# Performance work log

Measured on AMD Instinct MI355X. Metric: run time of the kernel, lower is better.

## Reference

```python
import jax, jax.numpy as jnp
import numpy as np

N_NODES = 100000
N_EDGES = 1600000
IN_DIM = 256
HID = 128
OUT_DIM = 2
N_LAYERS = 4
BN_EPS = 1e-5


def setup_inputs() -> dict:
    key = jax.random.key(0)
    ks = jax.random.split(key, 10)
    s_in = 1.0 / np.sqrt(IN_DIM)
    s_h = 1.0 / np.sqrt(HID)
    return {
        "x": jax.random.normal(ks[0], (N_NODES, IN_DIM), dtype=jnp.float32),
        "edge_index": jax.random.randint(ks[1], (2, N_EDGES), 0, N_NODES, dtype=jnp.int32),
        "W_in": jax.random.normal(ks[2], (IN_DIM, HID), dtype=jnp.float32) * s_in,
        "b_in": jnp.zeros((HID,), dtype=jnp.float32),
        # SAGEConv per-layer weights: lin_l (aggregated neighbors), lin_r (self/root)
        "W_l": jax.random.normal(ks[3], (N_LAYERS, HID, HID), dtype=jnp.float32) * s_h,
        "b_l": jnp.zeros((N_LAYERS, HID), dtype=jnp.float32),
        "W_r": jax.random.normal(ks[4], (N_LAYERS, HID, HID), dtype=jnp.float32) * s_h,
        "b_r": jnp.zeros((N_LAYERS, HID), dtype=jnp.float32),
        # BatchNorm (eval mode) params/buffers
        "bn_gamma": jnp.ones((N_LAYERS, HID), dtype=jnp.float32),
        "bn_beta": jnp.zeros((N_LAYERS, HID), dtype=jnp.float32),
        "bn_mean": jax.random.normal(ks[5], (N_LAYERS, HID), dtype=jnp.float32) * 0.01,
        "bn_var": jnp.ones((N_LAYERS, HID), dtype=jnp.float32),
        "W_cls": jax.random.normal(ks[6], (HID, OUT_DIM), dtype=jnp.float32) * s_h,
        "b_cls": jnp.zeros((OUT_DIM,), dtype=jnp.float32),
    }


def _sage_mean(h, src, dst, n):
    # gather source-node features along edges, scatter-mean at targets
    msg = h[src]  # [E, HID] -- the large irregular gather
    agg = jax.ops.segment_sum(msg, dst, num_segments=n)  # [N, HID]
    cnt = jax.ops.segment_sum(jnp.ones((src.shape[0],), h.dtype), dst, num_segments=n)
    return agg / jnp.maximum(cnt, 1.0)[:, None]


def reference(x, edge_index, W_in, b_in, W_l, b_l, W_r, b_r,
              bn_gamma, bn_beta, bn_mean, bn_var, W_cls, b_cls):
    n = x.shape[0]
    src, dst = edge_index[0], edge_index[1]
    h = jax.nn.relu(x @ W_in + b_in)  # dropout is identity at eval
    for i in range(N_LAYERS):
        h_in = h
        mean = _sage_mean(h, src, dst, n)
        h = mean @ W_l[i] + b_l[i] + h @ W_r[i] + b_r[i]
        # BatchNorm1d in eval mode (running stats)
        h = bn_gamma[i] * (h - bn_mean[i]) * jax.lax.rsqrt(bn_var[i] + BN_EPS) + bn_beta[i]
        h = jax.nn.relu(h)
        h = h + h_in
    return jax.nn.log_softmax(h @ W_cls + b_cls, axis=1)
```

## Files before the change

### kernel.cpp

```cpp
#include <hip/hip_runtime.h>

typedef unsigned int uint;
typedef unsigned short ushort;
typedef __attribute__((ext_vector_type(8))) short short8v;
typedef __attribute__((ext_vector_type(4))) float f32x4;

#define IN_DIM 256
#define HID 128
#define BN_EPS 1e-5f
#define NSHARD 8

__device__ __forceinline__ float bf2f(ushort u) { return __uint_as_float(((uint)u) << 16); }
__device__ __forceinline__ ushort f2bf(float f) {
    uint u = __float_as_uint(f);
    return (ushort)((u + 0x7fffu + ((u >> 16) & 1u)) >> 16);
}
__device__ __forceinline__ uint cvt_pk_bf16(float a, float b) {
    uint r;
    asm("v_cvt_pk_bf16_f32 %0, %1, %2" : "=v"(r) : "v"(a), "v"(b));
    return r;
}
__device__ __forceinline__ void gload_lds16(const void* g, void* l) {
    __builtin_amdgcn_global_load_lds(
        (const __attribute__((address_space(1))) uint*)g,
        (__attribute__((address_space(3))) uint*)l, 16, 0, 0);
}


__global__ void count_deg_kernel(const int* __restrict__ ei, int* __restrict__ deg, int E) {
    int e = blockIdx.x * blockDim.x + threadIdx.x;
    if (e < E) atomicAdd(&deg[ei[E + e]], 1);
}

#define SCAN_THREADS 256
#define SCAN_ELEMS 1024

__global__ __launch_bounds__(SCAN_THREADS) void scan1_kernel(const int* __restrict__ deg,
                                                             int* __restrict__ outp,
                                                             int* __restrict__ bsum, int n) {
    __shared__ int sdata[SCAN_THREADS];
    int t = threadIdx.x;
    int base = blockIdx.x * SCAN_ELEMS + t * 4;
    int v0 = 0, v1 = 0, v2 = 0, v3 = 0;
    if (base + 0 < n) v0 = deg[base + 0];
    if (base + 1 < n) v1 = deg[base + 1];
    if (base + 2 < n) v2 = deg[base + 2];
    if (base + 3 < n) v3 = deg[base + 3];
    int s = v0 + v1 + v2 + v3;
    sdata[t] = s;
    __syncthreads();
    int val = s;
    for (int off = 1; off < SCAN_THREADS; off <<= 1) {
        int add = (t >= off) ? sdata[t - off] : 0;
        __syncthreads();
        val += add;
        sdata[t] = val;
        __syncthreads();
    }
    int excl = val - s;
    if (base + 0 < n) outp[base + 0] = excl;
    if (base + 1 < n) outp[base + 1] = excl + v0;
    if (base + 2 < n) outp[base + 2] = excl + v0 + v1;
    if (base + 3 < n) outp[base + 3] = excl + v0 + v1 + v2;
    if (t == SCAN_THREADS - 1) bsum[blockIdx.x] = val;
}

__global__ void scan2_kernel(int* bsum, int nb) {
    if (threadIdx.x == 0 && blockIdx.x == 0) {
        int acc = 0;
        for (int i = 0; i < nb; i++) { int v = bsum[i]; bsum[i] = acc; acc += v; }
        bsum[nb] = acc;
    }
}

__global__ void scan3_kernel(int* __restrict__ row_ptr, const int* __restrict__ bsum, int n, int nb) {
    int i = blockIdx.x * blockDim.x + threadIdx.x;
    if (i < n) row_ptr[i] += bsum[i >> 10];
    else if (i == n) row_ptr[n] = bsum[nb];
}

__global__ __launch_bounds__(256) void fill_csr_sharded(const int* __restrict__ ei,
                                                        int* __restrict__ cursor,
                                                        int* __restrict__ esrc,
                                                        int E, int shardSize) {
    int s = blockIdx.x & (NSHARD - 1);
    int rank = blockIdx.x >> 3;
    int nteam = gridDim.x >> 3;
    int lo = s * shardSize;
    int hi = lo + shardSize;
    int stride = nteam * blockDim.x;
    for (int e = rank * blockDim.x + threadIdx.x; e < E; e += stride) {
        int d = ei[E + e];
        if (d >= lo && d < hi) {
            int pos = atomicAdd(&cursor[d], 1);
            esrc[pos] = ei[e];
        }
    }
}


__global__ __launch_bounds__(256) void pack_win(const float* __restrict__ W, ushort* __restrict__ Wt) {
    int idx = blockIdx.x * 256 + threadIdx.x;
    int k = idx >> 7, c = idx & 127;
    Wt[c * IN_DIM + k] = f2bf(W[idx]);
}

__global__ __launch_bounds__(256) void pack_wcat(const float* __restrict__ Wl,
                                                 const float* __restrict__ Wr,
                                                 ushort* __restrict__ Wt) {
    int idx = blockIdx.x * 256 + threadIdx.x;
    int layer = idx >> 15;
    int rem = idx & 32767;
    int k = rem >> 7, c = rem & 127;
    float v = (k < HID) ? Wl[layer * HID * HID + k * HID + c]
                        : Wr[layer * HID * HID + (k - HID) * HID + c];
    Wt[layer * (HID * 256) + c * 256 + k] = f2bf(v);
}


__global__ __launch_bounds__(256) void sage_mean_bf16(const ushort* __restrict__ h,
                                                      const int* __restrict__ row_ptr,
                                                      const int* __restrict__ esrc,
                                                      ushort* __restrict__ meanb, int n) {
    int node = blockIdx.x * 4 + (threadIdx.x >> 6);
    if (node >= n) return;
    int lane = threadIdx.x & 63;
    int start = row_ptr[node];
    int end = row_ptr[node + 1];
    float ax = 0.f, ay = 0.f;
    int j = start;
    for (; j + 15 < end; j += 16) {
        uint v[16];
        #pragma unroll
        for (int q = 0; q < 16; q++)
            v[q] = *(const uint*)(h + (size_t)esrc[j + q] * HID + lane * 2);
        #pragma unroll
        for (int q = 0; q < 16; q++) {
            ax += bf2f((ushort)(v[q] & 0xffffu));
            ay += bf2f((ushort)(v[q] >> 16));
        }
    }
    for (; j + 7 < end; j += 8) {
        uint v[8];
        #pragma unroll
        for (int q = 0; q < 8; q++)
            v[q] = *(const uint*)(h + (size_t)esrc[j + q] * HID + lane * 2);
        #pragma unroll
        for (int q = 0; q < 8; q++) {
            ax += bf2f((ushort)(v[q] & 0xffffu));
            ay += bf2f((ushort)(v[q] >> 16));
        }
    }
    for (; j < end; ++j) {
        uint v0 = *(const uint*)(h + (size_t)esrc[j] * HID + lane * 2);
        ax += bf2f((ushort)(v0 & 0xffffu));
        ay += bf2f((ushort)(v0 >> 16));
    }
    int deg = end - start;
    float inv = 1.0f / (float)(deg > 1 ? deg : 1);
    uint o = (uint)f2bf(ax * inv) | (((uint)f2bf(ay * inv)) << 16);
    *(uint*)(meanb + (size_t)node * HID + lane * 2) = o;
}


__global__ __launch_bounds__(256) void input_gemm_mfma(const float* __restrict__ x,
                                                       const ushort* __restrict__ Wt,
                                                       const float* __restrict__ b,
                                                       ushort* __restrict__ hout, int n) {
    __shared__ float Axs[32 * IN_DIM];
    int t = threadIdx.x;
    int l = t & 63;
    int wv = t >> 6;
    int colbase = wv * 32;
    int lr = l & 15;
    int grp = l >> 4;
    int ko = grp * 8;

    short8v Bf[8][2];
    #pragma unroll
    for (int ks = 0; ks < 8; ks++) {
        #pragma unroll
        for (int nt = 0; nt < 2; nt++) {
            int c = colbase + nt * 16 + lr;
            Bf[ks][nt] = *(const short8v*)(Wt + (size_t)c * IN_DIM + ks * 32 + ko);
        }
    }
    float bias0 = b[colbase + lr];
    float bias1 = b[colbase + 16 + lr];

    int ntiles = (n + 31) >> 5;
    for (int tile = blockIdx.x; tile < ntiles; tile += gridDim.x) {
        int row0 = tile * 32;
        __syncthreads();
        {
            const char* xb = (const char*)(x + (size_t)row0 * IN_DIM);
            char* lb = (char*)Axs;
            #pragma unroll
            for (int i = 0; i < 8; i++) {
                int off = i * 4096 + t * 16;
                int src = off ^ (((off >> 10) & 7) << 4);
                gload_lds16(xb + src, lb + i * 4096 + wv * 1024);
            }
        }
        __syncthreads();
        f32x4 acc00 = {0.f,0.f,0.f,0.f}, acc01 = {0.f,0.f,0.f,0.f};
        f32x4 acc10 = {0.f,0.f,0.f,0.f}, acc11 = {0.f,0.f,0.f,0.f};
        #pragma unroll
        for (int m = 0; m < 2; m++) {
            int r = m * 16 + lr;
            int rswz = (r & 7) << 4;
            const char* rowp = (const char*)Axs + r * 1024;
            short8v Af[8];
            #pragma unroll
            for (int ks = 0; ks < 8; ks++) {
                int kb = (ko + ks * 32) * 4;
                float4 p = *(const float4*)(rowp + (kb ^ rswz));
                float4 q = *(const float4*)(rowp + ((kb + 16) ^ rswz));
                union { uint4 u; short8v s; } cv;
                cv.u.x = cvt_pk_bf16(p.x, p.y);
                cv.u.y = cvt_pk_bf16(p.z, p.w);
                cv.u.z = cvt_pk_bf16(q.x, q.y);
                cv.u.w = cvt_pk_bf16(q.z, q.w);
                Af[ks] = cv.s;
            }
            if (m == 0) {
                #pragma unroll
                for (int ks = 0; ks < 8; ks++) {
                    acc00 = __builtin_amdgcn_mfma_f32_16x16x32_bf16(Af[ks], Bf[ks][0], acc00, 0, 0, 0);
                    acc01 = __builtin_amdgcn_mfma_f32_16x16x32_bf16(Af[ks], Bf[ks][1], acc01, 0, 0, 0);
                }
            } else {
                #pragma unroll
                for (int ks = 0; ks < 8; ks++) {
                    acc10 = __builtin_amdgcn_mfma_f32_16x16x32_bf16(Af[ks], Bf[ks][0], acc10, 0, 0, 0);
                    acc11 = __builtin_amdgcn_mfma_f32_16x16x32_bf16(Af[ks], Bf[ks][1], acc11, 0, 0, 0);
                }
            }
        }
        #pragma unroll
        for (int m = 0; m < 2; m++) {
            int rbase = row0 + m * 16 + grp * 4;
            f32x4 a0 = m == 0 ? acc00 : acc10;
            f32x4 a1 = m == 0 ? acc01 : acc11;
            #pragma unroll
            for (int r = 0; r < 4; r++) {
                int rowd = rbase + r;
                if (rowd < n) {
                    float z0 = a0[r] + bias0; z0 = z0 > 0.f ? z0 : 0.f;
                    float z1 = a1[r] + bias1; z1 = z1 > 0.f ? z1 : 0.f;
                    hout[(size_t)rowd * HID + colbase + lr] = f2bf(z0);
                    hout[(size_t)rowd * HID + colbase + 16 + lr] = f2bf(z1);
                }
            }
        }
    }
}


__global__ __launch_bounds__(256) void sage_layer_mfma(const ushort* __restrict__ h,
                                                       const ushort* __restrict__ mh,
                                                       ushort* __restrict__ hout,
                                                       const ushort* __restrict__ Wt,
                                                       const float* __restrict__ bl,
                                                       const float* __restrict__ br,
                                                       const float* __restrict__ gamma,
                                                       const float* __restrict__ beta,
                                                       const float* __restrict__ bmean,
                                                       const float* __restrict__ bvar,
                                                       int n) {
    __shared__ ushort Ams[64 * HID];
    __shared__ ushort Ahs[64 * HID];
    int t = threadIdx.x;
    int l = t & 63;
    int wv = t >> 6;
    int colbase = wv * 32;
    int lr = l & 15;
    int grp = l >> 4;
    int ko = grp * 8;

    short8v Bf[8][2];
    #pragma unroll
    for (int ks = 0; ks < 8; ks++) {
        #pragma unroll
        for (int nt = 0; nt < 2; nt++) {
            int c = colbase + nt * 16 + lr;
            Bf[ks][nt] = *(const short8v*)(Wt + (size_t)c * 256 + ks * 32 + ko);
        }
    }
    int c0 = colbase + lr;
    int c1 = c0 + 16;
    float scale0 = gamma[c0] * rsqrtf(bvar[c0] + BN_EPS);
    float scale1 = gamma[c1] * rsqrtf(bvar[c1] + BN_EPS);
    float shift0 = beta[c0] + (bl[c0] + br[c0] - bmean[c0]) * scale0;
    float shift1 = beta[c1] + (bl[c1] + br[c1] - bmean[c1]) * scale1;

    int ntiles = (n + 63) >> 6;
    for (int tile = blockIdx.x; tile < ntiles; tile += gridDim.x) {
        int row0 = tile * 64;
        __syncthreads();
        {
            const char* mb = (const char*)(mh + (size_t)row0 * HID);
            const char* hb = (const char*)(h + (size_t)row0 * HID);
            char* lm = (char*)Ams;
            char* lh = (char*)Ahs;
            #pragma unroll
            for (int i = 0; i < 4; i++) {
                int off = i * 4096 + t * 16;
                int src = off ^ (((off >> 8) & 7) << 4);
                gload_lds16(mb + src, lm + i * 4096 + wv * 1024);
                gload_lds16(hb + src, lh + i * 4096 + wv * 1024);
            }
        }
        __syncthreads();
        #pragma unroll
        for (int m = 0; m < 4; m++) {
            int r = m * 16 + lr;
            int rswz = (r & 7) << 4;
            const char* mrow = (const char*)Ams + r * 256;
            const char* hrow = (const char*)Ahs + r * 256;
            short8v Af[8];
            #pragma unroll
            for (int ks = 0; ks < 4; ks++) {
                int kb = (ko + ks * 32) * 2;
                Af[ks] = *(const short8v*)(mrow + (kb ^ rswz));
            }
            #pragma unroll
            for (int ks = 4; ks < 8; ks++) {
                int kb = (ko + (ks - 4) * 32) * 2;
                Af[ks] = *(const short8v*)(hrow + (kb ^ rswz));
            }
            f32x4 acc0 = {0.f,0.f,0.f,0.f};
            f32x4 acc1 = {0.f,0.f,0.f,0.f};
            #pragma unroll
            for (int ks = 0; ks < 8; ks++) {
                acc0 = __builtin_amdgcn_mfma_f32_16x16x32_bf16(Af[ks], Bf[ks][0], acc0, 0, 0, 0);
                acc1 = __builtin_amdgcn_mfma_f32_16x16x32_bf16(Af[ks], Bf[ks][1], acc1, 0, 0, 0);
            }
            int rbase = m * 16 + grp * 4;
            #pragma unroll
            for (int r2 = 0; r2 < 4; r2++) {
                int rloc = rbase + r2;
                int rowd = row0 + rloc;
                if (rowd < n) {
                    int rs = (rloc & 7) << 4;
                    float res0 = bf2f(*(const ushort*)((const char*)Ahs + rloc * 256 + ((c0 * 2) ^ rs)));
                    float res1 = bf2f(*(const ushort*)((const char*)Ahs + rloc * 256 + ((c1 * 2) ^ rs)));
                    float z0 = acc0[r2] * scale0 + shift0; z0 = z0 > 0.f ? z0 : 0.f;
                    float z1 = acc1[r2] * scale1 + shift1; z1 = z1 > 0.f ? z1 : 0.f;
                    hout[(size_t)rowd * HID + c0] = f2bf(z0 + res0);
                    hout[(size_t)rowd * HID + c1] = f2bf(z1 + res1);
                }
            }
        }
    }
}


__global__ __launch_bounds__(256) void classifier_bf16(const ushort* __restrict__ h,
                                                       const float* __restrict__ Wc,
                                                       const float* __restrict__ bc,
                                                       float* __restrict__ outp, int n) {
    __shared__ float Wcs[HID * 2];
    int t = threadIdx.x;
    if (t < 64) *(float4*)&Wcs[t * 4] = *(const float4*)&Wc[t * 4];
    __syncthreads();
    int rowInBlk = t >> 4;
    int sub = t & 15;
    int row = blockIdx.x * 16 + rowInBlk;
    float l0 = 0.f, l1 = 0.f;
    if (row < n) {
        const ushort* hr = h + (size_t)row * HID + sub * 8;
        uint4 v = *(const uint4*)hr;
        float e0 = bf2f((ushort)(v.x & 0xffffu)), e1 = bf2f((ushort)(v.x >> 16));
        float e2 = bf2f((ushort)(v.y & 0xffffu)), e3 = bf2f((ushort)(v.y >> 16));
        float e4 = bf2f((ushort)(v.z & 0xffffu)), e5 = bf2f((ushort)(v.z >> 16));
        float e6 = bf2f((ushort)(v.w & 0xffffu)), e7 = bf2f((ushort)(v.w >> 16));
        int k0 = sub * 8;
        l0 += e0 * Wcs[(k0 + 0) * 2] + e1 * Wcs[(k0 + 1) * 2] + e2 * Wcs[(k0 + 2) * 2] + e3 * Wcs[(k0 + 3) * 2];
        l0 += e4 * Wcs[(k0 + 4) * 2] + e5 * Wcs[(k0 + 5) * 2] + e6 * Wcs[(k0 + 6) * 2] + e7 * Wcs[(k0 + 7) * 2];
        l1 += e0 * Wcs[(k0 + 0) * 2 + 1] + e1 * Wcs[(k0 + 1) * 2 + 1] + e2 * Wcs[(k0 + 2) * 2 + 1] + e3 * Wcs[(k0 + 3) * 2 + 1];
        l1 += e4 * Wcs[(k0 + 4) * 2 + 1] + e5 * Wcs[(k0 + 5) * 2 + 1] + e6 * Wcs[(k0 + 6) * 2 + 1] + e7 * Wcs[(k0 + 7) * 2 + 1];
    }
    #pragma unroll
    for (int off = 1; off < 16; off <<= 1) {
        l0 += __shfl_xor(l0, off);
        l1 += __shfl_xor(l1, off);
    }
    if (sub == 0 && row < n) {
        l0 += bc[0];
        l1 += bc[1];
        float m = fmaxf(l0, l1);
        float lse = m + logf(expf(l0 - m) + expf(l1 - m));
        outp[(size_t)row * 2 + 0] = l0 - lse;
        outp[(size_t)row * 2 + 1] = l1 - lse;
    }
}


extern "C" void kernel_launch(void* const* d_in, const int* in_sizes, int n_in,
                              void* d_out, int out_size, void* d_ws, size_t ws_size,
                              hipStream_t stream) {
    const float* x     = (const float*)d_in[0];
    const int*   ei    = (const int*)d_in[1];
    const float* W_in  = (const float*)d_in[2];
    const float* b_in  = (const float*)d_in[3];
    const float* W_l   = (const float*)d_in[4];
    const float* b_l   = (const float*)d_in[5];
    const float* W_r   = (const float*)d_in[6];
    const float* b_r   = (const float*)d_in[7];
    const float* bn_g  = (const float*)d_in[8];
    const float* bn_b  = (const float*)d_in[9];
    const float* bn_m  = (const float*)d_in[10];
    const float* bn_v  = (const float*)d_in[11];
    const float* W_cls = (const float*)d_in[12];
    const float* b_cls = (const float*)d_in[13];
    float* outp = (float*)d_out;

    const int N = in_sizes[0] / IN_DIM;
    const int E = in_sizes[1] / 2;

    char* w = (char*)d_ws;
    const size_t HB = (size_t)N * HID * sizeof(ushort);
    ushort* hA     = (ushort*)(w);
    ushort* hB     = (ushort*)(w + HB);
    ushort* meanb  = (ushort*)(w + 2 * HB);
    ushort* Wt_in  = (ushort*)(w + 3 * HB);
    ushort* WcatT  = (ushort*)(w + 3 * HB + 65536);
    char*  ints    = w + 3 * HB + 65536 + 262144;
    int*   row_ptr = (int*)(ints);
    int*   cursor  = (int*)(ints + 400128);
    int*   bsum    = (int*)(ints + 800256);
    int*   esrc    = (int*)(ints + 801280);

    const int nbScan = (N + SCAN_ELEMS - 1) / SCAN_ELEMS;
    const int shardSize = (N + NSHARD - 1) / NSHARD;

    pack_win<<<128, 256, 0, stream>>>(W_in, Wt_in);
    pack_wcat<<<512, 256, 0, stream>>>(W_l, W_r, WcatT);

    hipMemsetAsync(cursor, 0, (size_t)N * sizeof(int), stream);
    count_deg_kernel<<<(E + 255) / 256, 256, 0, stream>>>(ei, cursor, E);
    scan1_kernel<<<nbScan, SCAN_THREADS, 0, stream>>>(cursor, row_ptr, bsum, N);
    scan2_kernel<<<1, 64, 0, stream>>>(bsum, nbScan);
    scan3_kernel<<<(N + 256) / 256, 256, 0, stream>>>(row_ptr, bsum, N, nbScan);
    hipMemcpyAsync(cursor, row_ptr, (size_t)N * sizeof(int), hipMemcpyDeviceToDevice, stream);
    fill_csr_sharded<<<2048, 256, 0, stream>>>(ei, cursor, esrc, E, shardSize);

    input_gemm_mfma<<<(N + 31) / 32, 256, 0, stream>>>(x, Wt_in, b_in, hA, N);

    ushort* hcur = hA;
    ushort* hoth = hB;
    for (int i = 0; i < 4; i++) {
        sage_mean_bf16<<<(N + 3) / 4, 256, 0, stream>>>(hcur, row_ptr, esrc, meanb, N);
        sage_layer_mfma<<<(N + 63) / 64, 256, 0, stream>>>(hcur, meanb, hoth,
                                                  WcatT + (size_t)i * HID * 256,
                                                  b_l + i * HID, b_r + i * HID,
                                                  bn_g + i * HID, bn_b + i * HID,
                                                  bn_m + i * HID, bn_v + i * HID, N);
        ushort* tmp = hcur; hcur = hoth; hoth = tmp;
    }

    classifier_bf16<<<(N + 15) / 16, 256, 0, stream>>>(hcur, W_cls, b_cls, outp, N);
}
```

Measured before the change: 580.4 us.

## Replace atomic CSR build with two-level bucketed counting sort

The CSR construction no longer uses global degree atomics, a three-kernel scan, a memcpy and a sharded atomic fill. It now histograms destinations into 512-node buckets per edge chunk, scans those counts in one block, and partitions edges into buckets with LDS atomics. Each bucket then builds its own row_ptr slice and sorted source list in shared memory. The aim is fewer global atomics and launches and more local scatter, at the cost of an extra 8-byte-per-edge staging buffer, a single-block serial scan over 256 chunks, and a different within-row edge order.

```diff
diff --git a/kernel.cpp b/kernel.cpp
--- a/kernel.cpp
+++ b/kernel.cpp
@@ -8,7 +8,6 @@
 #define IN_DIM 256
 #define HID 128
 #define BN_EPS 1e-5f
-#define NSHARD 8
 
 __device__ __forceinline__ float bf2f(ushort u) { return __uint_as_float(((uint)u) << 16); }
 __device__ __forceinline__ ushort f2bf(float f) {
@@ -27,73 +26,121 @@
 }
 
 
-__global__ void count_deg_kernel(const int* __restrict__ ei, int* __restrict__ deg, int E) {
-    int e = blockIdx.x * blockDim.x + threadIdx.x;
-    if (e < E) atomicAdd(&deg[ei[E + e]], 1);
-}
-
-#define SCAN_THREADS 256
-#define SCAN_ELEMS 1024
-
-__global__ __launch_bounds__(SCAN_THREADS) void scan1_kernel(const int* __restrict__ deg,
-                                                             int* __restrict__ outp,
-                                                             int* __restrict__ bsum, int n) {
-    __shared__ int sdata[SCAN_THREADS];
-    int t = threadIdx.x;
-    int base = blockIdx.x * SCAN_ELEMS + t * 4;
-    int v0 = 0, v1 = 0, v2 = 0, v3 = 0;
-    if (base + 0 < n) v0 = deg[base + 0];
-    if (base + 1 < n) v1 = deg[base + 1];
-    if (base + 2 < n) v2 = deg[base + 2];
-    if (base + 3 < n) v3 = deg[base + 3];
-    int s = v0 + v1 + v2 + v3;
-    sdata[t] = s;
-    __syncthreads();
-    int val = s;
-    for (int off = 1; off < SCAN_THREADS; off <<= 1) {
-        int add = (t >= off) ? sdata[t - off] : 0;
-        __syncthreads();
-        val += add;
-        sdata[t] = val;
-        __syncthreads();
-    }
-    int excl = val - s;
-    if (base + 0 < n) outp[base + 0] = excl;
-    if (base + 1 < n) outp[base + 1] = excl + v0;
-    if (base + 2 < n) outp[base + 2] = excl + v0 + v1;
-    if (base + 3 < n) outp[base + 3] = excl + v0 + v1 + v2;
-    if (t == SCAN_THREADS - 1) bsum[blockIdx.x] = val;
-}
-
-__global__ void scan2_kernel(int* bsum, int nb) {
-    if (threadIdx.x == 0 && blockIdx.x == 0) {
-        int acc = 0;
-        for (int i = 0; i < nb; i++) { int v = bsum[i]; bsum[i] = acc; acc += v; }
-        bsum[nb] = acc;
-    }
-}
-
-__global__ void scan3_kernel(int* __restrict__ row_ptr, const int* __restrict__ bsum, int n, int nb) {
-    int i = blockIdx.x * blockDim.x + threadIdx.x;
-    if (i < n) row_ptr[i] += bsum[i >> 10];
-    else if (i == n) row_ptr[n] = bsum[nb];
-}
-
-__global__ __launch_bounds__(256) void fill_csr_sharded(const int* __restrict__ ei,
-                                                        int* __restrict__ cursor,
-                                                        int* __restrict__ esrc,
-                                                        int E, int shardSize) {
-    int s = blockIdx.x & (NSHARD - 1);
-    int rank = blockIdx.x >> 3;
-    int nteam = gridDim.x >> 3;
-    int lo = s * shardSize;
-    int hi = lo + shardSize;
-    int stride = nteam * blockDim.x;
-    for (int e = rank * blockDim.x + threadIdx.x; e < E; e += stride) {
-        int d = ei[E + e];
-        if (d >= lo && d < hi) {
-            int pos = atomicAdd(&cursor[d], 1);
-            esrc[pos] = ei[e];
+__global__ __launch_bounds__(256) void hist_kernel(const int* __restrict__ ei,
+                                                   int* __restrict__ histG,
+                                                   int E, int chunk) {
+    __shared__ int hcnt[256];
+    int t = threadIdx.x;
+    hcnt[t] = 0;
+    __syncthreads();
+    int e0 = blockIdx.x * chunk;
+    int e1 = min(E, e0 + chunk);
+    for (int e = e0 + t; e < e1; e += 256)
+        atomicAdd(&hcnt[__builtin_nontemporal_load(ei + E + e) >> 9], 1);
+    __syncthreads();
+    histG[blockIdx.x * 256 + t] = hcnt[t];
+}
+
+__global__ __launch_bounds__(256) void basescan_kernel(const int* __restrict__ histG,
+                                                       int* __restrict__ baseG,
+                                                       int* __restrict__ bucketStart,
+                                                       int nchunk, int nbuck, int E) {
+    __shared__ int sA[256], sB[256];
+    int t = threadIdx.x;
+    int tot = 0;
+    for (int c = 0; c < nchunk; c++) tot += histG[c * 256 + t];
+    sA[t] = tot;
+    __syncthreads();
+    int* src = sA; int* dst = sB;
+    for (int off = 1; off < 256; off <<= 1) {
+        int v = src[t];
+        if (t >= off) v += src[t - off];
+        dst[t] = v;
+        __syncthreads();
+        int* tmp = src; src = dst; dst = tmp;
+    }
+    int excl = src[t] - tot;
+    if (t < nbuck) bucketStart[t] = excl;
+    if (t == 0) bucketStart[nbuck] = E;
+    int running = excl;
+    for (int c = 0; c < nchunk; c++) {
+        baseG[c * 256 + t] = running;
+        running += histG[c * 256 + t];
+    }
+}
+
+__global__ __launch_bounds__(256) void partition_kernel(const int* __restrict__ ei,
+                                                        const int* __restrict__ baseG,
+                                                        uint2* __restrict__ ebuck,
+                                                        int E, int chunk) {
+    __shared__ int cur[256];
+    int t = threadIdx.x;
+    cur[t] = baseG[blockIdx.x * 256 + t];
+    __syncthreads();
+    int e0 = blockIdx.x * chunk;
+    int e1 = min(E, e0 + chunk);
+    for (int e = e0 + t; e < e1; e += 256) {
+        int d = __builtin_nontemporal_load(ei + E + e);
+        int s = __builtin_nontemporal_load(ei + e);
+        int pos = atomicAdd(&cur[d >> 9], 1);
+        ebuck[pos] = make_uint2((uint)s, (uint)d);
+    }
+}
+
+__global__ __launch_bounds__(256) void bucket_build(const uint2* __restrict__ ebuck,
+                                                    const int* __restrict__ bucketStart,
+                                                    int* __restrict__ row_ptr,
+                                                    int* __restrict__ esrc,
+                                                    int n, int nbuck) {
+    __shared__ int deg[512];
+    __shared__ int sA[512], sB[512];
+    __shared__ int cur[512];
+    __shared__ int img[16384];
+    int b = blockIdx.x;
+    int t = threadIdx.x;
+    int lo = b << 9;
+    int hi = min(n, lo + 512);
+    int nn = hi - lo;
+    int eStart = bucketStart[b];
+    int eEnd = bucketStart[b + 1];
+    int cnt = eEnd - eStart;
+    for (int i = t; i < 512; i += 256) deg[i] = 0;
+    __syncthreads();
+    for (int e = eStart + t; e < eEnd; e += 256) {
+        uint2 p = ebuck[e];
+        atomicAdd(&deg[(int)p.y - lo], 1);
+    }
+    __syncthreads();
+    for (int i = t; i < 512; i += 256) sA[i] = deg[i];
+    __syncthreads();
+    int* src = sA; int* dst = sB;
+    for (int off = 1; off < 512; off <<= 1) {
+        for (int i = t; i < 512; i += 256) {
+            int v = src[i];
+            if (i >= off) v += src[i - off];
+            dst[i] = v;
+        }
+        __syncthreads();
+        int* tmp = src; src = dst; dst = tmp;
+    }
+    for (int i = t; i < 512; i += 256) cur[i] = src[i] - deg[i];
+    __syncthreads();
+    for (int i = t; i < nn; i += 256) row_ptr[lo + i] = eStart + cur[i];
+    if (b == nbuck - 1 && t == 0) row_ptr[n] = eEnd;
+    __syncthreads();
+    if (cnt <= 16384) {
+        for (int e = eStart + t; e < eEnd; e += 256) {
+            uint2 p = ebuck[e];
+            int pos = atomicAdd(&cur[(int)p.y - lo], 1);
+            img[pos] = (int)p.x;
+        }
+        __syncthreads();
+        for (int i = t; i < cnt; i += 256) esrc[eStart + i] = img[i];
+    } else {
+        for (int e = eStart + t; e < eEnd; e += 256) {
+            uint2 p = ebuck[e];
+            int pos = atomicAdd(&cur[(int)p.y - lo], 1);
+            esrc[eStart + pos] = (int)p.x;
         }
     }
 }
@@ -426,25 +473,25 @@
     ushort* meanb  = (ushort*)(w + 2 * HB);
     ushort* Wt_in  = (ushort*)(w + 3 * HB);
     ushort* WcatT  = (ushort*)(w + 3 * HB + 65536);
-    char*  ints    = w + 3 * HB + 65536 + 262144;
-    int*   row_ptr = (int*)(ints);
-    int*   cursor  = (int*)(ints + 400128);
-    int*   bsum    = (int*)(ints + 800256);
-    int*   esrc    = (int*)(ints + 801280);
-
-    const int nbScan = (N + SCAN_ELEMS - 1) / SCAN_ELEMS;
-    const int shardSize = (N + NSHARD - 1) / NSHARD;
+    size_t off = 3 * HB + 65536 + 262144;
+    int* row_ptr = (int*)(w + off);  off += ((size_t)(N + 1) * 4 + 255) & ~(size_t)255;
+    int* esrc    = (int*)(w + off);  off += (size_t)E * 4;
+    uint2* ebuck = (uint2*)(w + off); off += (size_t)E * 8;
+    int* histG   = (int*)(w + off);  off += 256 * 256 * 4;
+    int* baseG   = (int*)(w + off);  off += 256 * 256 * 4;
+    int* bucketStart = (int*)(w + off); off += 4096;
+
+    const int nbuck = (N + 511) >> 9;
+    const int nchunk = 256;
+    const int chunk = (E + nchunk - 1) / nchunk;
 
     pack_win<<<128, 256, 0, stream>>>(W_in, Wt_in);
     pack_wcat<<<512, 256, 0, stream>>>(W_l, W_r, WcatT);
 
-    hipMemsetAsync(cursor, 0, (size_t)N * sizeof(int), stream);
-    count_deg_kernel<<<(E + 255) / 256, 256, 0, stream>>>(ei, cursor, E);
-    scan1_kernel<<<nbScan, SCAN_THREADS, 0, stream>>>(cursor, row_ptr, bsum, N);
-    scan2_kernel<<<1, 64, 0, stream>>>(bsum, nbScan);
-    scan3_kernel<<<(N + 256) / 256, 256, 0, stream>>>(row_ptr, bsum, N, nbScan);
-    hipMemcpyAsync(cursor, row_ptr, (size_t)N * sizeof(int), hipMemcpyDeviceToDevice, stream);
-    fill_csr_sharded<<<2048, 256, 0, stream>>>(ei, cursor, esrc, E, shardSize);
+    hist_kernel<<<nchunk, 256, 0, stream>>>(ei, histG, E, chunk);
+    basescan_kernel<<<1, 256, 0, stream>>>(histG, baseG, bucketStart, nchunk, nbuck, E);
+    partition_kernel<<<nchunk, 256, 0, stream>>>(ei, baseG, ebuck, E, chunk);
+    bucket_build<<<nbuck, 256, 0, stream>>>(ebuck, bucketStart, row_ptr, esrc, N, nbuck);
 
     input_gemm_mfma<<<(N + 31) / 32, 256, 0, stream>>>(x, Wt_in, b_in, hA, N);
 
```

Result: faster. 529.5 us, median of 2 (-8.8%).
